# Performance work log

Hardware: AMD Instinct MI355X
Metric: run time of the kernel (lower is better)

## Reference

```python
import jax, jax.numpy as jnp
import numpy as np

N = 100000
E = 1600000
F_IN = 64
DIM = 64
OUT = 2
BN_EPS = 1e-5


def setup_inputs() -> dict:
    key = jax.random.key(0)
    ks = jax.random.split(key, 12)
    s = lambda fan_in: 1.0 / np.sqrt(fan_in)
    inp = {
        "x": jax.random.normal(ks[0], (N, F_IN), dtype=jnp.float32),
        "edge_index": jax.random.randint(ks[1], (2, E), 0, N, dtype=jnp.int64),
        # conv1 MLP: Linear(F_IN, DIM) -> ReLU -> Linear(DIM, DIM)
        "W1a": jax.random.uniform(ks[2], (F_IN, DIM), jnp.float32, -s(F_IN), s(F_IN)),
        "b1a": jnp.zeros((DIM,), jnp.float32),
        "W1b": jax.random.uniform(ks[3], (DIM, DIM), jnp.float32, -s(DIM), s(DIM)),
        "b1b": jnp.zeros((DIM,), jnp.float32),
        "g1": jnp.ones((DIM,), jnp.float32),
        "be1": jnp.zeros((DIM,), jnp.float32),
        # conv5 MLP: Linear(DIM, DIM) -> ReLU -> Linear(DIM, 2)
        "W5a": jax.random.uniform(ks[4], (DIM, DIM), jnp.float32, -s(DIM), s(DIM)),
        "b5a": jnp.zeros((DIM,), jnp.float32),
        "W5b": jax.random.uniform(ks[5], (DIM, OUT), jnp.float32, -s(DIM), s(DIM)),
        "b5b": jnp.zeros((OUT,), jnp.float32),
        "g5": jnp.ones((OUT,), jnp.float32),
        "be5": jnp.zeros((OUT,), jnp.float32),
    }
    return inp


def _gin_agg(x, src, dst):
    # GINConv with eps=0: (1+eps)*x + sum_{j in N(i)} x_j
    agg = jax.ops.segment_sum(x[src], dst, num_segments=N)
    return x + agg


def _batchnorm(h, gamma, beta):
    mu = jnp.mean(h, axis=0)
    var = jnp.var(h, axis=0)  # biased, as torch BN uses for normalization
    return (h - mu) * jax.lax.rsqrt(var + BN_EPS) * gamma + beta


def reference(x, edge_index, W1a, b1a, W1b, b1b, g1, be1,
              W5a, b5a, W5b, b5b, g5, be5):
    src, dst = edge_index[0], edge_index[1]
    # conv1
    h = _gin_agg(x, src, dst)                      # [N, F_IN]
    h = jax.nn.relu(h @ W1a + b1a) @ W1b + b1b     # [N, DIM]
    h = jax.nn.relu(h)
    h = _batchnorm(h, g1, be1)
    # conv5
    h = _gin_agg(h, src, dst)                      # [N, DIM]
    h = jax.nn.relu(h @ W5a + b5a) @ W5b + b5b     # [N, OUT]
    h = jax.nn.relu(h)
    h = _batchnorm(h, g5, be5)
    return h
```

## Files before the change

kernel.cpp:

```cpp
#include <hip/hip_runtime.h>

#define NN 100000
#define FD 64
#define OUTF 2
#define NB 391
#define NBP 392
#define P1CH 4096
#define NTILE 6250
#define MLPB 782
#define GPSTR 800

typedef short bf16x8 __attribute__((ext_vector_type(8), may_alias));
typedef float f32x4 __attribute__((ext_vector_type(4)));
typedef float f32x2 __attribute__((ext_vector_type(2)));

__device__ inline ushort f2bf(float f) {
    uint u = __float_as_uint(f);
    uint r = (u + 0x7FFFu + ((u >> 16) & 1u)) >> 16;
    return (ushort)r;
}
__device__ inline float bf2f(ushort v) {
    return __uint_as_float(((uint)v) << 16);
}


__global__ void k_zero(float* __restrict__ p, int n) {
    int i = blockIdx.x * blockDim.x + threadIdx.x;
    if (i < n) p[i] = 0.f;
}

__global__ void k_copy4(const float4* __restrict__ s, float4* __restrict__ d, int n4) {
    int i = blockIdx.x * blockDim.x + threadIdx.x;
    int st = gridDim.x * blockDim.x;
    for (; i < n4; i += st) d[i] = s[i];
}

__global__ void k_cvt(const float4* __restrict__ x4, ushort4* __restrict__ xb4, int n4) {
    int i = blockIdx.x * blockDim.x + threadIdx.x;
    int st = gridDim.x * blockDim.x;
    for (; i < n4; i += st) {
        float4 v = x4[i];
        ushort4 w;
        w.x = f2bf(v.x);
        w.y = f2bf(v.y);
        w.z = f2bf(v.z);
        w.w = f2bf(v.w);
        xb4[i] = w;
    }
}

__global__ __launch_bounds__(256) void k_cvt_hist(
        const int* __restrict__ ei, int* __restrict__ ghist, int E_, int np1,
        const float4* __restrict__ x4, ushort4* __restrict__ xb4,
        ushort* __restrict__ xb, ushort* __restrict__ h1b, int n4) {
    __shared__ int h[NB];
    int tid = threadIdx.x;
    int blk = blockIdx.x;
    if (blk < np1) {
        for (int i = tid; i < NB; i += 256) h[i] = 0;
        __syncthreads();
        int c0 = blk * P1CH;
        int c1 = min(c0 + P1CH, E_);
        for (int i = c0 + tid; i < c1; i += 256) {
            int d = ei[E_ + i];
            int b = min(max(d >> 8, 0), NB - 1);
            atomicAdd(&h[b], 1);
        }
        __syncthreads();
        int* row = ghist + (size_t)blk * NBP;
        for (int i = tid; i < NB; i += 256) row[i] = h[i];
    } else {
        int bb = blk - np1;
        if (bb == 0 && tid < 16) {
            ushort4 z = {0, 0, 0, 0};
            ((ushort4*)(xb + (size_t)NN * FD))[tid] = z;
            ((ushort4*)(h1b + (size_t)NN * FD))[tid] = z;
        }
        int i = bb * 256 + tid;
        int st = 2048 * 256;
        for (; i < n4; i += st) {
            float4 v = x4[i];
            ushort4 w;
            w.x = f2bf(v.x);
            w.y = f2bf(v.y);
            w.z = f2bf(v.z);
            w.w = f2bf(v.w);
            xb4[i] = w;
        }
    }
}


__global__ __launch_bounds__(512) void k_scanCol(int* __restrict__ ghist,
                                                 int* __restrict__ tot, int np1) {
    __shared__ int ts[512];
    int b = blockIdx.x;
    int tid = threadIdx.x;
    int v = (tid < np1) ? ghist[(size_t)tid * NBP + b] : 0;
    ts[tid] = v;
    __syncthreads();
    for (int off = 1; off < 512; off <<= 1) {
        int u = (tid >= off) ? ts[tid - off] : 0;
        __syncthreads();
        ts[tid] += u;
        __syncthreads();
    }
    if (tid < np1) ghist[(size_t)tid * NBP + b] = ts[tid] - v;
    if (tid == 511) tot[b] = ts[511];
}

__global__ __launch_bounds__(512) void k_scanB2(const int* __restrict__ tot,
                                                int* __restrict__ bbase,
                                                float* __restrict__ S) {
    __shared__ int ts[512];
    int tid = threadIdx.x;
    if (tid < 192) S[tid] = 0.f;
    int v = (tid < NB) ? tot[tid] : 0;
    ts[tid] = v;
    __syncthreads();
    for (int off = 1; off < 512; off <<= 1) {
        int u = (tid >= off) ? ts[tid - off] : 0;
        __syncthreads();
        ts[tid] += u;
        __syncthreads();
    }
    if (tid < NB) bbase[tid] = ts[tid] - v;
    if (tid == 511) bbase[NB] = ts[511];
}

__global__ __launch_bounds__(256) void k_p1b2(const int* __restrict__ ei,
                                              const int* __restrict__ ghist,
                                              const int* __restrict__ bbase,
                                              int* __restrict__ part, int E_) {
    __shared__ int cur[NB];
    int tid = threadIdx.x;
    const int* row = ghist + (size_t)blockIdx.x * NBP;
    for (int i = tid; i < NB; i += 256) cur[i] = bbase[i] + row[i];
    __syncthreads();
    int c0 = blockIdx.x * P1CH;
    int c1 = min(c0 + P1CH, E_);
    for (int i = c0 + tid; i < c1; i += 256) {
        int s = ei[i];
        int d = ei[E_ + i];
        int b = min(max(d >> 8, 0), NB - 1);
        int slot = atomicAdd(&cur[b], 1);
        part[slot] = ((d & 255) << 20) | (s & 0xFFFFF);
    }
}

__global__ __launch_bounds__(256) void k_build(const int* __restrict__ part,
                                               const int* __restrict__ bbase,
                                               int* __restrict__ rowptr,
                                               int* __restrict__ csr, int E_) {
    __shared__ int cnt[256];
    __shared__ int ts[256];
    __shared__ int cur[256];
    int b = blockIdx.x;
    int tid = threadIdx.x;
    cnt[tid] = 0;
    __syncthreads();
    int s0 = bbase[b], s1 = bbase[b + 1];
    for (int i = s0 + tid; i < s1; i += 256) {
        int v = part[i];
        atomicAdd(&cnt[(v >> 20) & 255], 1);
    }
    __syncthreads();
    int v = cnt[tid];
    ts[tid] = v;
    __syncthreads();
    for (int off = 1; off < 256; off <<= 1) {
        int u = (tid >= off) ? ts[tid - off] : 0;
        __syncthreads();
        ts[tid] += u;
        __syncthreads();
    }
    int excl = ts[tid] - v;
    int node = b * 256 + tid;
    if (node < NN) rowptr[node] = s0 + excl;
    cur[tid] = s0 + excl;
    if (b == 0 && tid == 0) rowptr[NN] = E_;
    __syncthreads();
    for (int i = s0 + tid; i < s1; i += 256) {
        int v2 = part[i];
        int lj = (v2 >> 20) & 255;
        int pos = atomicAdd(&cur[lj], 1);
        csr[pos] = v2 & 0xFFFFF;
    }
}


#define GSTEP(T, A01, A23)                                                     \
    {                                                                          \
        int s = __shfl(id, (T) * 4 + g);                                       \
        uint2 v = *(const uint2*)(Xb + ((long)s << 6) + (l << 2));             \
        f32x2 p, q2;                                                           \
        p[0] = __uint_as_float(v.x << 16);                                     \
        p[1] = __uint_as_float(v.x & 0xFFFF0000u);                             \
        q2[0] = __uint_as_float(v.y << 16);                                    \
        q2[1] = __uint_as_float(v.y & 0xFFFF0000u);                            \
        A01 += p;                                                              \
        A23 += q2;                                                             \
    }

__global__ __launch_bounds__(256) void k_gather2(
        const ushort* __restrict__ Xb, const int* __restrict__ rowptr,
        const int* __restrict__ csr,
        const float* __restrict__ bs, const float* __restrict__ bq,
        const float* __restrict__ gam, const float* __restrict__ bet,
        ushort* __restrict__ outb, int affine) {
    int tid = threadIdx.x;
    int lane = tid & 63;
    int n = (blockIdx.x * blockDim.x + tid) >> 6;
    if (n >= NN) return;
    int g = lane >> 4;
    int l = lane & 15;
    int start = rowptr[n], end = rowptr[n + 1];
    int deg = end - start;

    f32x2 a01 = {0.f, 0.f}, a23 = {0.f, 0.f};
    f32x2 b01 = {0.f, 0.f}, b23 = {0.f, 0.f};
    if (g == 0) {
        uint2 v = *(const uint2*)(Xb + ((long)n << 6) + (l << 2));
        a01[0] = __uint_as_float(v.x << 16);
        a01[1] = __uint_as_float(v.x & 0xFFFF0000u);
        a23[0] = __uint_as_float(v.y << 16);
        a23[1] = __uint_as_float(v.y & 0xFFFF0000u);
    }

    for (int base = start; base < end; base += 64) {
        int cnt = min(end - base, 64);
        int id = NN;
        if (lane < cnt) id = csr[base + lane];
        int nsteps = (cnt + 3) >> 2;
        int t = 0;
        for (; t + 4 <= nsteps; t += 4) {
            GSTEP(t + 0, a01, a23)
            GSTEP(t + 1, b01, b23)
            GSTEP(t + 2, a01, a23)
            GSTEP(t + 3, b01, b23)
        }
        for (; t + 2 <= nsteps; t += 2) {
            GSTEP(t + 0, a01, a23)
            GSTEP(t + 1, b01, b23)
        }
        if (t < nsteps) GSTEP(t, a01, a23)
    }
    a01 += b01;
    a23 += b23;
    float A[4] = {a01[0], a01[1], a23[0], a23[1]};
#pragma unroll
    for (int c = 0; c < 4; c++) {
        float v = A[c];
        v += __shfl_xor(v, 16);
        v += __shfl_xor(v, 32);
        A[c] = v;
    }

    if (g == 0) {
        if (affine) {
            float dp1 = (float)(deg + 1);
#pragma unroll
            for (int c = 0; c < 4; c++) {
                int ch = l * 4 + c;
                float mu = bs[ch] * (1.f / NN);
                float var = bq[ch] * (1.f / NN) - mu * mu;
                float s = gam[ch] * rsqrtf(var + 1e-5f);
                float sh = fmaf(-mu, s, bet[ch]);
                A[c] = fmaf(A[c], s, dp1 * sh);
            }
        }
        ushort4 v;
        v.x = f2bf(A[0]); v.y = f2bf(A[1]); v.z = f2bf(A[2]); v.w = f2bf(A[3]);
        ((ushort4*)(outb + ((long)n << 6)))[l] = v;
    }
}


__global__ __launch_bounds__(256) void k_mlp1_mfma(
        const ushort* __restrict__ Ab,
        const float* __restrict__ Wa, const float* __restrict__ ba,
        const float* __restrict__ Wb, const float* __restrict__ bb,
        ushort* __restrict__ H, float* __restrict__ gp1s, float* __restrict__ gp1q) {
    __shared__ __attribute__((aligned(16))) short tile[4][16 * 72];
    __shared__ float sArr[64], qArr[64];
    int tid = threadIdx.x;
    int w = tid >> 6, lane = tid & 63;
    int l = lane & 15, quad = lane >> 4;
    if (tid < 64) { sArr[tid] = 0.f; qArr[tid] = 0.f; }
    __syncthreads();

    bf16x8 B1[2][4], B2[2][4];
#pragma unroll
    for (int ks = 0; ks < 2; ks++)
#pragma unroll
        for (int t = 0; t < 4; t++) {
            bf16x8 f1, f2;
#pragma unroll
            for (int j = 0; j < 8; j++) {
                int k = ks * 32 + quad * 8 + j;
                f1[j] = (short)f2bf(Wa[k * 64 + t * 16 + l]);
                f2[j] = (short)f2bf(Wb[k * 64 + t * 16 + l]);
            }
            B1[ks][t] = f1;
            B2[ks][t] = f2;
        }
    float bias1[4], bias2[4];
#pragma unroll
    for (int t = 0; t < 4; t++) {
        bias1[t] = ba[t * 16 + l];
        bias2[t] = bb[t * 16 + l];
    }

    float s[4] = {0.f, 0.f, 0.f, 0.f}, q[4] = {0.f, 0.f, 0.f, 0.f};
    short* tp = &tile[w][0];
    int gw = blockIdx.x * 4 + w;
    int nw = gridDim.x * 4;
    bf16x8 A0, A1;
    if (gw < NTILE) {
        int m0 = gw * 16;
        A0 = *(const bf16x8*)(Ab + (size_t)(m0 + l) * FD + quad * 8);
        A1 = *(const bf16x8*)(Ab + (size_t)(m0 + l) * FD + 32 + quad * 8);
    }
    for (int tau = gw; tau < NTILE; tau += nw) {
        int m0 = tau * 16;
        int nxt = tau + nw;
        bf16x8 nA0, nA1;
        if (nxt < NTILE) {
            int nm0 = nxt * 16;
            nA0 = *(const bf16x8*)(Ab + (size_t)(nm0 + l) * FD + quad * 8);
            nA1 = *(const bf16x8*)(Ab + (size_t)(nm0 + l) * FD + 32 + quad * 8);
        }
#pragma unroll
        for (int t = 0; t < 4; t++) {
            f32x4 c = {0.f, 0.f, 0.f, 0.f};
            c = __builtin_amdgcn_mfma_f32_16x16x32_bf16(A0, B1[0][t], c, 0, 0, 0);
            c = __builtin_amdgcn_mfma_f32_16x16x32_bf16(A1, B1[1][t], c, 0, 0, 0);
#pragma unroll
            for (int r = 0; r < 4; r++) {
                float v = fmaxf(c[r] + bias1[t], 0.f);
                tp[(quad * 4 + r) * 72 + t * 16 + l] = (short)f2bf(v);
            }
        }
        bf16x8 A20 = *(const bf16x8*)&tp[l * 72 + quad * 8];
        bf16x8 A21 = *(const bf16x8*)&tp[l * 72 + 32 + quad * 8];
#pragma unroll
        for (int t = 0; t < 4; t++) {
            f32x4 c = {0.f, 0.f, 0.f, 0.f};
            c = __builtin_amdgcn_mfma_f32_16x16x32_bf16(A20, B2[0][t], c, 0, 0, 0);
            c = __builtin_amdgcn_mfma_f32_16x16x32_bf16(A21, B2[1][t], c, 0, 0, 0);
#pragma unroll
            for (int r = 0; r < 4; r++) {
                float v = fmaxf(c[r] + bias2[t], 0.f);
                s[t] += v;
                q[t] += v * v;
                tp[(quad * 4 + r) * 72 + t * 16 + l] = (short)f2bf(v);
            }
        }
        int row = lane >> 2, ch = lane & 3;
        bf16x8 o0 = *(const bf16x8*)&tp[row * 72 + ch * 16];
        bf16x8 o1 = *(const bf16x8*)&tp[row * 72 + ch * 16 + 8];
        *(bf16x8*)(H + (size_t)(m0 + row) * FD + ch * 16) = o0;
        *(bf16x8*)(H + (size_t)(m0 + row) * FD + ch * 16 + 8) = o1;
        A0 = nA0;
        A1 = nA1;
    }
#pragma unroll
    for (int t = 0; t < 4; t++) {
        s[t] += __shfl_xor(s[t], 16); s[t] += __shfl_xor(s[t], 32);
        q[t] += __shfl_xor(q[t], 16); q[t] += __shfl_xor(q[t], 32);
    }
    if (quad == 0) {
#pragma unroll
        for (int t = 0; t < 4; t++) {
            atomicAdd(&sArr[t * 16 + l], s[t]);
            atomicAdd(&qArr[t * 16 + l], q[t]);
        }
    }
    __syncthreads();
    if (tid < 64) {
        gp1s[tid * GPSTR + blockIdx.x] = sArr[tid];
        gp1q[tid * GPSTR + blockIdx.x] = qArr[tid];
    }
}

__global__ __launch_bounds__(256) void k_red1(const float* __restrict__ gp1s,
                                              const float* __restrict__ gp1q,
                                              float* __restrict__ gsum,
                                              float* __restrict__ gsq, int nb) {
    __shared__ float rs[256], rq[256];
    int ch = blockIdx.x;
    int tid = threadIdx.x;
    float s = 0.f, q = 0.f;
    for (int k = tid; k < nb; k += 256) {
        s += gp1s[ch * GPSTR + k];
        q += gp1q[ch * GPSTR + k];
    }
    rs[tid] = s;
    rq[tid] = q;
    __syncthreads();
    for (int off = 128; off > 0; off >>= 1) {
        if (tid < off) {
            rs[tid] += rs[tid + off];
            rq[tid] += rq[tid + off];
        }
        __syncthreads();
    }
    if (tid == 0) {
        gsum[ch] = rs[0];
        gsq[ch] = rq[0];
    }
}

__global__ __launch_bounds__(256) void k_mlp2_mfma(
        const ushort* __restrict__ Ab,
        const float* __restrict__ Wa, const float* __restrict__ ba,
        const float* __restrict__ Wb2, const float* __restrict__ bb2,
        float* __restrict__ O, float* __restrict__ gsum, float* __restrict__ gsq) {
    __shared__ __attribute__((aligned(16))) short tile[4][16 * 72];
    __shared__ float sArr[2], qArr[2];
    int tid = threadIdx.x;
    int w = tid >> 6, lane = tid & 63;
    int l = lane & 15, quad = lane >> 4;
    if (tid < 2) { sArr[tid] = 0.f; qArr[tid] = 0.f; }
    __syncthreads();

    bf16x8 B1[2][4], B2[2];
#pragma unroll
    for (int ks = 0; ks < 2; ks++) {
#pragma unroll
        for (int t = 0; t < 4; t++) {
            bf16x8 f1;
#pragma unroll
            for (int j = 0; j < 8; j++) {
                int k = ks * 32 + quad * 8 + j;
                f1[j] = (short)f2bf(Wa[k * 64 + t * 16 + l]);
            }
            B1[ks][t] = f1;
        }
        bf16x8 f2;
#pragma unroll
        for (int j = 0; j < 8; j++) {
            int k = ks * 32 + quad * 8 + j;
            f2[j] = (l < OUTF) ? (short)f2bf(Wb2[k * OUTF + l]) : (short)0;
        }
        B2[ks] = f2;
    }
    float bias1[4];
#pragma unroll
    for (int t = 0; t < 4; t++) bias1[t] = ba[t * 16 + l];
    float bias2 = (l < OUTF) ? bb2[l] : 0.f;

    float s = 0.f, q = 0.f;
    short* tp = &tile[w][0];
    int gw = blockIdx.x * 4 + w;
    int nw = gridDim.x * 4;
    bf16x8 A0, A1;
    if (gw < NTILE) {
        int m0 = gw * 16;
        A0 = *(const bf16x8*)(Ab + (size_t)(m0 + l) * FD + quad * 8);
        A1 = *(const bf16x8*)(Ab + (size_t)(m0 + l) * FD + 32 + quad * 8);
    }
    for (int tau = gw; tau < NTILE; tau += nw) {
        int m0 = tau * 16;
        int nxt = tau + nw;
        bf16x8 nA0, nA1;
        if (nxt < NTILE) {
            int nm0 = nxt * 16;
            nA0 = *(const bf16x8*)(Ab + (size_t)(nm0 + l) * FD + quad * 8);
            nA1 = *(const bf16x8*)(Ab + (size_t)(nm0 + l) * FD + 32 + quad * 8);
        }
#pragma unroll
        for (int t = 0; t < 4; t++) {
            f32x4 c = {0.f, 0.f, 0.f, 0.f};
            c = __builtin_amdgcn_mfma_f32_16x16x32_bf16(A0, B1[0][t], c, 0, 0, 0);
            c = __builtin_amdgcn_mfma_f32_16x16x32_bf16(A1, B1[1][t], c, 0, 0, 0);
#pragma unroll
            for (int r = 0; r < 4; r++) {
                float v = fmaxf(c[r] + bias1[t], 0.f);
                tp[(quad * 4 + r) * 72 + t * 16 + l] = (short)f2bf(v);
            }
        }
        bf16x8 A20 = *(const bf16x8*)&tp[l * 72 + quad * 8];
        bf16x8 A21 = *(const bf16x8*)&tp[l * 72 + 32 + quad * 8];
        f32x4 c = {0.f, 0.f, 0.f, 0.f};
        c = __builtin_amdgcn_mfma_f32_16x16x32_bf16(A20, B2[0], c, 0, 0, 0);
        c = __builtin_amdgcn_mfma_f32_16x16x32_bf16(A21, B2[1], c, 0, 0, 0);
#pragma unroll
        for (int r = 0; r < 4; r++) {
            float v = fmaxf(c[r] + bias2, 0.f);
            if (l < OUTF) {
                s += v;
                q += v * v;
                O[(size_t)(m0 + quad * 4 + r) * OUTF + l] = v;
            }
        }
        A0 = nA0;
        A1 = nA1;
    }
    s += __shfl_xor(s, 16); s += __shfl_xor(s, 32);
    q += __shfl_xor(q, 16); q += __shfl_xor(q, 32);
    if (quad == 0 && l < OUTF) {
        atomicAdd(&sArr[l], s);
        atomicAdd(&qArr[l], q);
    }
    __syncthreads();
    if (tid < OUTF) {
        atomicAdd(&gsum[tid], sArr[tid]);
        atomicAdd(&gsq[tid], qArr[tid]);
    }
}

template <bool BF16OUT>
__global__ __launch_bounds__(256) void k_mlp64(
        const float* __restrict__ X,
        const float* __restrict__ Wa, const float* __restrict__ ba,
        const float* __restrict__ Wb, const float* __restrict__ bb,
        void* __restrict__ Hv, float* __restrict__ gsum, float* __restrict__ gsq) {
    __shared__ float row[256 * 65];
    int tid = threadIdx.x;
    long node = (long)blockIdx.x * 256 + tid;
    bool valid = node < NN;
    if (valid) {
        const float4* rp = (const float4*)(X + node * FD);
#pragma unroll
        for (int q = 0; q < 16; q++) {
            float4 v = rp[q];
            row[tid * 65 + 4 * q + 0] = v.x;
            row[tid * 65 + 4 * q + 1] = v.y;
            row[tid * 65 + 4 * q + 2] = v.z;
            row[tid * 65 + 4 * q + 3] = v.w;
        }
    }
    float acc[64];
#pragma unroll
    for (int j = 0; j < 64; j++) acc[j] = ba[j];
    if (valid) {
        for (int k = 0; k < 64; k++) {
            float xv = row[tid * 65 + k];
            const float* wr = Wa + k * 64;
#pragma unroll
            for (int j = 0; j < 64; j++) acc[j] = fmaf(xv, wr[j], acc[j]);
        }
    }
#pragma unroll
    for (int j = 0; j < 64; j++) row[tid * 65 + j] = fmaxf(acc[j], 0.f);
#pragma unroll
    for (int j = 0; j < 64; j++) acc[j] = bb[j];
    if (valid) {
        for (int k = 0; k < 64; k++) {
            float xv = row[tid * 65 + k];
            const float* wr = Wb + k * 64;
#pragma unroll
            for (int j = 0; j < 64; j++) acc[j] = fmaf(xv, wr[j], acc[j]);
        }
    }
#pragma unroll
    for (int j = 0; j < 64; j++) {
        float v = valid ? fmaxf(acc[j], 0.f) : 0.f;
        row[tid * 65 + j] = v;
    }
    if (valid) {
        if (BF16OUT) {
            ushort4* op = (ushort4*)((ushort*)Hv + node * FD);
#pragma unroll
            for (int q = 0; q < 16; q++) {
                ushort4 w;
                w.x = f2bf(row[tid * 65 + 4 * q + 0]);
                w.y = f2bf(row[tid * 65 + 4 * q + 1]);
                w.z = f2bf(row[tid * 65 + 4 * q + 2]);
                w.w = f2bf(row[tid * 65 + 4 * q + 3]);
                op[q] = w;
            }
        } else {
            float4* op = (float4*)((float*)Hv + node * FD);
#pragma unroll
            for (int q = 0; q < 16; q++) {
                float4 v;
                v.x = row[tid * 65 + 4 * q + 0];
                v.y = row[tid * 65 + 4 * q + 1];
                v.z = row[tid * 65 + 4 * q + 2];
                v.w = row[tid * 65 + 4 * q + 3];
                op[q] = v;
            }
        }
    }
    __syncthreads();
    if (tid < 64) {
        float s = 0.f, q = 0.f;
        for (int r = 0; r < 256; r++) {
            float v = row[r * 65 + tid];
            s += v;
            q += v * v;
        }
        atomicAdd(&gsum[tid], s);
        atomicAdd(&gsq[tid], q);
    }
}

__global__ __launch_bounds__(256) void k_mlp_out(
        const float* __restrict__ X,
        const float* __restrict__ Wa, const float* __restrict__ ba,
        const float* __restrict__ Wb, const float* __restrict__ bb,
        float* __restrict__ O, float* __restrict__ gsum, float* __restrict__ gsq) {
    __shared__ float row[256 * 65];
    __shared__ float red[256][4];
    int tid = threadIdx.x;
    long node = (long)blockIdx.x * 256 + tid;
    bool valid = node < NN;
    if (valid) {
        const float4* rp = (const float4*)(X + node * FD);
#pragma unroll
        for (int q = 0; q < 16; q++) {
            float4 v = rp[q];
            row[tid * 65 + 4 * q + 0] = v.x;
            row[tid * 65 + 4 * q + 1] = v.y;
            row[tid * 65 + 4 * q + 2] = v.z;
            row[tid * 65 + 4 * q + 3] = v.w;
        }
    }
    float acc[64];
#pragma unroll
    for (int j = 0; j < 64; j++) acc[j] = ba[j];
    if (valid) {
        for (int k = 0; k < 64; k++) {
            float xv = row[tid * 65 + k];
            const float* wr = Wa + k * 64;
#pragma unroll
            for (int j = 0; j < 64; j++) acc[j] = fmaf(xv, wr[j], acc[j]);
        }
    }
#pragma unroll
    for (int j = 0; j < 64; j++) row[tid * 65 + j] = fmaxf(acc[j], 0.f);
    float a0 = bb[0];
    float a1 = bb[1];
    if (valid) {
        for (int k = 0; k < 64; k++) {
            float xv = row[tid * 65 + k];
            a0 = fmaf(xv, Wb[k * 2 + 0], a0);
            a1 = fmaf(xv, Wb[k * 2 + 1], a1);
        }
    }
    float v0 = valid ? fmaxf(a0, 0.f) : 0.f;
    float v1 = valid ? fmaxf(a1, 0.f) : 0.f;
    if (valid) {
        float2 v;
        v.x = v0;
        v.y = v1;
        ((float2*)O)[node] = v;
    }
    red[tid][0] = v0;
    red[tid][1] = v0 * v0;
    red[tid][2] = v1;
    red[tid][3] = v1 * v1;
    __syncthreads();
    for (int off = 128; off > 0; off >>= 1) {
        if (tid < off) {
#pragma unroll
            for (int c = 0; c < 4; c++) red[tid][c] += red[tid + off][c];
        }
        __syncthreads();
    }
    if (tid == 0) {
        atomicAdd(&gsum[0], red[0][0]);
        atomicAdd(&gsq[0], red[0][1]);
        atomicAdd(&gsum[1], red[0][2]);
        atomicAdd(&gsq[1], red[0][3]);
    }
}


__global__ void k_bnfin(const float* __restrict__ gsum, const float* __restrict__ gsq,
                        const float* __restrict__ g, const float* __restrict__ be,
                        float* __restrict__ sc, float* __restrict__ sh, int C, float invN) {
    int c = threadIdx.x;
    if (c < C) {
        float mu = gsum[c] * invN;
        float var = gsq[c] * invN - mu * mu;
        float s = g[c] * rsqrtf(var + 1e-5f);
        sc[c] = s;
        sh[c] = fmaf(-mu, s, be[c]);
    }
}

__global__ void k_bnfin_apply2(const float* __restrict__ gsum,
                               const float* __restrict__ gsq,
                               const float* __restrict__ g,
                               const float* __restrict__ be,
                               float* __restrict__ o, int n) {
    int i = blockIdx.x * blockDim.x + threadIdx.x;
    if (i < n) {
        int c = i & 1;
        float mu = gsum[c] * (1.f / NN);
        float var = gsq[c] * (1.f / NN) - mu * mu;
        float s = g[c] * rsqrtf(var + 1e-5f);
        float sh = fmaf(-mu, s, be[c]);
        o[i] = fmaf(o[i], s, sh);
    }
}

__global__ void k_bn_apply2(float* __restrict__ o, const float* __restrict__ sc,
                            const float* __restrict__ sh, int n) {
    int i = blockIdx.x * blockDim.x + threadIdx.x;
    if (i < n) {
        int c = i & 1;
        o[i] = fmaf(o[i], sc[c], sh[c]);
    }
}


__global__ void k_scatter(const float* __restrict__ x, const int* __restrict__ ei,
                          float* __restrict__ agg, int E_) {
    int lane = threadIdx.x & 63;
    int wid = (blockIdx.x * blockDim.x + threadIdx.x) >> 6;
    int nw = (gridDim.x * blockDim.x) >> 6;
    for (long e = wid; e < E_; e += nw) {
        int s = ei[e];
        int d = ei[E_ + e];
        float v = x[(long)s * FD + lane];
        atomicAdd(&agg[(long)d * FD + lane], v);
    }
}

__global__ void k_scatter_bn(const float* __restrict__ h, const int* __restrict__ ei,
                             const float* __restrict__ sc, const float* __restrict__ sh,
                             float* __restrict__ agg, int E_) {
    int lane = threadIdx.x & 63;
    float scl = sc[lane];
    float shf = sh[lane];
    int wid = (blockIdx.x * blockDim.x + threadIdx.x) >> 6;
    int nw = (gridDim.x * blockDim.x) >> 6;
    for (long e = wid; e < E_; e += nw) {
        int s = ei[e];
        int d = ei[E_ + e];
        float v = fmaf(h[(long)s * FD + lane], scl, shf);
        atomicAdd(&agg[(long)d * FD + lane], v);
    }
}

__global__ void k_bn_copy(const float4* __restrict__ h, const float4* __restrict__ sc4,
                          const float4* __restrict__ sh4, float4* __restrict__ o, int n4) {
    int i = blockIdx.x * blockDim.x + threadIdx.x;
    int st = gridDim.x * blockDim.x;
    for (; i < n4; i += st) {
        float4 v = h[i];
        int c = i & 15;
        float4 s = sc4[c];
        float4 b = sh4[c];
        v.x = fmaf(v.x, s.x, b.x);
        v.y = fmaf(v.y, s.y, b.y);
        v.z = fmaf(v.z, s.z, b.z);
        v.w = fmaf(v.w, s.w, b.w);
        o[i] = v;
    }
}


extern "C" void kernel_launch(void* const* d_in, const int* in_sizes, int n_in,
                              void* d_out, int out_size, void* d_ws, size_t ws_size,
                              hipStream_t stream) {
    const float* x   = (const float*)d_in[0];
    const int*   ei  = (const int*)d_in[1];
    const float* W1a = (const float*)d_in[2];
    const float* b1a = (const float*)d_in[3];
    const float* W1b = (const float*)d_in[4];
    const float* b1b = (const float*)d_in[5];
    const float* g1  = (const float*)d_in[6];
    const float* be1 = (const float*)d_in[7];
    const float* W5a = (const float*)d_in[8];
    const float* b5a = (const float*)d_in[9];
    const float* W5b = (const float*)d_in[10];
    const float* b5b = (const float*)d_in[11];
    const float* g5  = (const float*)d_in[12];
    const float* be5 = (const float*)d_in[13];
    float* out = (float*)d_out;

    const int E = in_sizes[1] / 2;

    float* ws = (float*)d_ws;
    float* agg = ws;
    ushort* aggb = (ushort*)ws;
    float* gp1s = ws + 3200000;
    float* gp1q = ws + 3260000;
    ushort* xb  = (ushort*)(ws + 6400000);
    ushort* h1b = (ushort*)(ws + 9600032);
    float* h1_fb = ws + 6400000;
    float* S   = ws + 12800064;
    float* gsum1  = S;
    float* gsq1   = S + 64;
    float* gsum2  = S + 128;
    float* gsq2   = S + 160;
    float* scale1 = S + 192;
    float* shift1 = S + 256;
    float* scale2 = S + 320;
    float* shift2 = S + 328;

    int* ibase  = (int*)(S + 512);
    int* rowptr = ibase;
    int* csr    = ibase + 100004;
    int* bbase  = ibase + 100004 + E;
    int* tot    = bbase + 400;
    int* ghist  = tot + 392;
    int* part   = (int*)agg;

    const int np1 = (E + P1CH - 1) / P1CH;
    size_t needed = (size_t)(12800064 + 512) * 4 +
                    (size_t)(100004 + E + 400 + 392 + (size_t)np1 * NBP) * 4;

    const int n4 = NN * FD / 4;
    const int nblk = (NN + 255) / 256;

    if (ws_size >= needed && np1 <= 512) {
        k_cvt_hist<<<np1 + 2048, 256, 0, stream>>>(ei, ghist, E, np1, (const float4*)x,
                                                   (ushort4*)xb, xb, h1b, n4);
        k_scanCol<<<NB, 512, 0, stream>>>(ghist, tot, np1);
        k_scanB2<<<1, 512, 0, stream>>>(tot, bbase, S);
        k_p1b2<<<np1, 256, 0, stream>>>(ei, ghist, bbase, part, E);
        k_build<<<NB, 256, 0, stream>>>(part, bbase, rowptr, csr, E);

        k_gather2<<<25000, 256, 0, stream>>>(xb, rowptr, csr, nullptr, nullptr,
                                             nullptr, nullptr, aggb, 0);
        k_mlp1_mfma<<<MLPB, 256, 0, stream>>>(aggb, W1a, b1a, W1b, b1b, h1b, gp1s, gp1q);
        k_red1<<<64, 256, 0, stream>>>(gp1s, gp1q, gsum1, gsq1, MLPB);
        k_gather2<<<25000, 256, 0, stream>>>(h1b, rowptr, csr, gsum1, gsq1,
                                             g1, be1, aggb, 1);
        k_mlp2_mfma<<<MLPB, 256, 0, stream>>>(aggb, W5a, b5a, W5b, b5b, out, gsum2, gsq2);
        k_bnfin_apply2<<<(NN * OUTF + 255) / 256, 256, 0, stream>>>(gsum2, gsq2, g5, be5,
                                                                    out, NN * OUTF);
    } else {
        k_zero<<<1, 256, 0, stream>>>(S, 192);
        k_copy4<<<4096, 256, 0, stream>>>((const float4*)x, (float4*)agg, n4);
        k_scatter<<<4096, 256, 0, stream>>>(x, ei, agg, E);
        k_mlp64<false><<<nblk, 256, 0, stream>>>(agg, W1a, b1a, W1b, b1b,
                                                 (void*)h1_fb, gsum1, gsq1);
        k_bnfin<<<1, 64, 0, stream>>>(gsum1, gsq1, g1, be1, scale1, shift1, 64, 1.f / NN);
        k_bn_copy<<<4096, 256, 0, stream>>>((const float4*)h1_fb, (const float4*)scale1,
                                            (const float4*)shift1, (float4*)agg, n4);
        k_scatter_bn<<<4096, 256, 0, stream>>>(h1_fb, ei, scale1, shift1, agg, E);
        k_mlp_out<<<nblk, 256, 0, stream>>>(agg, W5a, b5a, W5b, b5b, out, gsum2, gsq2);
        k_bnfin<<<1, 64, 0, stream>>>(gsum2, gsq2, g5, be5, scale2, shift2, OUTF, 1.f / NN);
        k_bn_apply2<<<(NN * OUTF + 255) / 256, 256, 0, stream>>>(out, scale2, shift2, NN * OUTF);
    }
}
```

Baseline: 263.3 us.

## Fold scan and BN reductions into last-block epilogues; stage bucket edges in LDS

Removes two small kernel launches (k_scanB2 and k_red1) by having the last finishing block of k_scanCol and k_mlp1_mfma, detected through an atomic counter with thread fences, perform the global scan and the per-channel BN reduction. The counters are zeroed in k_cvt_hist. k_build now caches each bucket's edges in a 24KB LDS buffer so the second pass reads LDS instead of global memory. The trade-off is a serialized tail in one block and more LDS per block, which may lower occupancy in k_build.

```diff
diff --git a/kernel.cpp b/kernel.cpp
--- a/kernel.cpp
+++ b/kernel.cpp
@@ -9,6 +9,7 @@
 #define NTILE 6250
 #define MLPB 782
 #define GPSTR 800
+#define BCAP 6016
 
 typedef short bf16x8 __attribute__((ext_vector_type(8), may_alias));
 typedef float f32x4 __attribute__((ext_vector_type(4)));
@@ -52,7 +53,8 @@
 __global__ __launch_bounds__(256) void k_cvt_hist(
         const int* __restrict__ ei, int* __restrict__ ghist, int E_, int np1,
         const float4* __restrict__ x4, ushort4* __restrict__ xb4,
-        ushort* __restrict__ xb, ushort* __restrict__ h1b, int n4) {
+        ushort* __restrict__ xb, ushort* __restrict__ h1b,
+        int* __restrict__ ctrs, int n4) {
     __shared__ int h[NB];
     int tid = threadIdx.x;
     int blk = blockIdx.x;
@@ -76,6 +78,10 @@
             ((ushort4*)(xb + (size_t)NN * FD))[tid] = z;
             ((ushort4*)(h1b + (size_t)NN * FD))[tid] = z;
         }
+        if (bb == 0 && tid == 16) {
+            ctrs[0] = 0;
+            ctrs[1] = 0;
+        }
         int i = bb * 256 + tid;
         int st = 2048 * 256;
         for (; i < n4; i += st) {
@@ -90,10 +96,13 @@
     }
 }
 
-
 __global__ __launch_bounds__(512) void k_scanCol(int* __restrict__ ghist,
-                                                 int* __restrict__ tot, int np1) {
+                                                 int* __restrict__ tot, int np1,
+                                                 int* __restrict__ bbase,
+                                                 float* __restrict__ S,
+                                                 int* __restrict__ ctr) {
     __shared__ int ts[512];
+    __shared__ int isLast;
     int b = blockIdx.x;
     int tid = threadIdx.x;
     int v = (tid < np1) ? ghist[(size_t)tid * NBP + b] : 0;
@@ -107,16 +116,17 @@
     }
     if (tid < np1) ghist[(size_t)tid * NBP + b] = ts[tid] - v;
     if (tid == 511) tot[b] = ts[511];
-}
-
-__global__ __launch_bounds__(512) void k_scanB2(const int* __restrict__ tot,
-                                                int* __restrict__ bbase,
-                                                float* __restrict__ S) {
-    __shared__ int ts[512];
-    int tid = threadIdx.x;
+    __syncthreads();
+    if (tid == 0) {
+        __threadfence();
+        isLast = (atomicAdd(ctr, 1) == NB - 1);
+    }
+    __syncthreads();
+    if (!isLast) return;
+    __threadfence();
     if (tid < 192) S[tid] = 0.f;
-    int v = (tid < NB) ? tot[tid] : 0;
-    ts[tid] = v;
+    int v2 = (tid < NB) ? tot[tid] : 0;
+    ts[tid] = v2;
     __syncthreads();
     for (int off = 1; off < 512; off <<= 1) {
         int u = (tid >= off) ? ts[tid - off] : 0;
@@ -124,7 +134,7 @@
         ts[tid] += u;
         __syncthreads();
     }
-    if (tid < NB) bbase[tid] = ts[tid] - v;
+    if (tid < NB) bbase[tid] = ts[tid] - v2;
     if (tid == 511) bbase[NB] = ts[511];
 }
 
@@ -155,14 +165,25 @@
     __shared__ int cnt[256];
     __shared__ int ts[256];
     __shared__ int cur[256];
+    __shared__ int ebuf[BCAP];
     int b = blockIdx.x;
     int tid = threadIdx.x;
     cnt[tid] = 0;
     __syncthreads();
     int s0 = bbase[b], s1 = bbase[b + 1];
-    for (int i = s0 + tid; i < s1; i += 256) {
-        int v = part[i];
-        atomicAdd(&cnt[(v >> 20) & 255], 1);
+    int len = s1 - s0;
+    bool inLds = (len <= BCAP);
+    if (inLds) {
+        for (int i = tid; i < len; i += 256) {
+            int v = part[s0 + i];
+            ebuf[i] = v;
+            atomicAdd(&cnt[(v >> 20) & 255], 1);
+        }
+    } else {
+        for (int i = tid; i < len; i += 256) {
+            int v = part[s0 + i];
+            atomicAdd(&cnt[(v >> 20) & 255], 1);
+        }
     }
     __syncthreads();
     int v = cnt[tid];
@@ -180,11 +201,20 @@
     cur[tid] = s0 + excl;
     if (b == 0 && tid == 0) rowptr[NN] = E_;
     __syncthreads();
-    for (int i = s0 + tid; i < s1; i += 256) {
-        int v2 = part[i];
-        int lj = (v2 >> 20) & 255;
-        int pos = atomicAdd(&cur[lj], 1);
-        csr[pos] = v2 & 0xFFFFF;
+    if (inLds) {
+        for (int i = tid; i < len; i += 256) {
+            int v2 = ebuf[i];
+            int lj = (v2 >> 20) & 255;
+            int pos = atomicAdd(&cur[lj], 1);
+            csr[pos] = v2 & 0xFFFFF;
+        }
+    } else {
+        for (int i = tid; i < len; i += 256) {
+            int v2 = part[s0 + i];
+            int lj = (v2 >> 20) & 255;
+            int pos = atomicAdd(&cur[lj], 1);
+            csr[pos] = v2 & 0xFFFFF;
+        }
     }
 }
 
@@ -280,9 +310,12 @@
         const ushort* __restrict__ Ab,
         const float* __restrict__ Wa, const float* __restrict__ ba,
         const float* __restrict__ Wb, const float* __restrict__ bb,
-        ushort* __restrict__ H, float* __restrict__ gp1s, float* __restrict__ gp1q) {
+        ushort* __restrict__ H, float* __restrict__ gp1s, float* __restrict__ gp1q,
+        float* __restrict__ gsum, float* __restrict__ gsq, int* __restrict__ ctr) {
     __shared__ __attribute__((aligned(16))) short tile[4][16 * 72];
     __shared__ float sArr[64], qArr[64];
+    __shared__ float rs[256], rq[256];
+    __shared__ int isLast;
     int tid = threadIdx.x;
     int w = tid >> 6, lane = tid & 63;
     int l = lane & 15, quad = lane >> 4;
@@ -381,33 +414,26 @@
         gp1s[tid * GPSTR + blockIdx.x] = sArr[tid];
         gp1q[tid * GPSTR + blockIdx.x] = qArr[tid];
     }
-}
-
-__global__ __launch_bounds__(256) void k_red1(const float* __restrict__ gp1s,
-                                              const float* __restrict__ gp1q,
-                                              float* __restrict__ gsum,
-                                              float* __restrict__ gsq, int nb) {
-    __shared__ float rs[256], rq[256];
-    int ch = blockIdx.x;
-    int tid = threadIdx.x;
-    float s = 0.f, q = 0.f;
-    for (int k = tid; k < nb; k += 256) {
-        s += gp1s[ch * GPSTR + k];
-        q += gp1q[ch * GPSTR + k];
-    }
-    rs[tid] = s;
-    rq[tid] = q;
-    __syncthreads();
-    for (int off = 128; off > 0; off >>= 1) {
-        if (tid < off) {
-            rs[tid] += rs[tid + off];
-            rq[tid] += rq[tid + off];
-        }
-        __syncthreads();
-    }
+    __syncthreads();
     if (tid == 0) {
-        gsum[ch] = rs[0];
-        gsq[ch] = rq[0];
+        __threadfence();
+        isLast = (atomicAdd(ctr, 1) == (int)gridDim.x - 1);
+    }
+    __syncthreads();
+    if (!isLast) return;
+    __threadfence();
+    int ch = tid & 63, seg = tid >> 6;
+    float ss = 0.f, qq = 0.f;
+    for (int k = seg; k < MLPB; k += 4) {
+        ss += gp1s[ch * GPSTR + k];
+        qq += gp1q[ch * GPSTR + k];
+    }
+    rs[tid] = ss;
+    rq[tid] = qq;
+    __syncthreads();
+    if (tid < 64) {
+        gsum[ch] = rs[tid] + rs[tid + 64] + rs[tid + 128] + rs[tid + 192];
+        gsq[ch] = rq[tid] + rq[tid + 64] + rq[tid + 128] + rq[tid + 192];
     }
 }
 
@@ -798,6 +824,7 @@
     int* rowptr = ibase;
     int* csr    = ibase + 100004;
     int* bbase  = ibase + 100004 + E;
+    int* ctrs   = bbase + 396;
     int* tot    = bbase + 400;
     int* ghist  = tot + 392;
     int* part   = (int*)agg;
@@ -811,16 +838,15 @@
 
     if (ws_size >= needed && np1 <= 512) {
         k_cvt_hist<<<np1 + 2048, 256, 0, stream>>>(ei, ghist, E, np1, (const float4*)x,
-                                                   (ushort4*)xb, xb, h1b, n4);
-        k_scanCol<<<NB, 512, 0, stream>>>(ghist, tot, np1);
-        k_scanB2<<<1, 512, 0, stream>>>(tot, bbase, S);
+                                                   (ushort4*)xb, xb, h1b, ctrs, n4);
+        k_scanCol<<<NB, 512, 0, stream>>>(ghist, tot, np1, bbase, S, &ctrs[0]);
         k_p1b2<<<np1, 256, 0, stream>>>(ei, ghist, bbase, part, E);
         k_build<<<NB, 256, 0, stream>>>(part, bbase, rowptr, csr, E);
 
         k_gather2<<<25000, 256, 0, stream>>>(xb, rowptr, csr, nullptr, nullptr,
                                              nullptr, nullptr, aggb, 0);
-        k_mlp1_mfma<<<MLPB, 256, 0, stream>>>(aggb, W1a, b1a, W1b, b1b, h1b, gp1s, gp1q);
-        k_red1<<<64, 256, 0, stream>>>(gp1s, gp1q, gsum1, gsq1, MLPB);
+        k_mlp1_mfma<<<MLPB, 256, 0, stream>>>(aggb, W1a, b1a, W1b, b1b, h1b,
+                                              gp1s, gp1q, gsum1, gsq1, &ctrs[1]);
         k_gather2<<<25000, 256, 0, stream>>>(h1b, rowptr, csr, gsum1, gsq1,
                                              g1, be1, aggb, 1);
         k_mlp2_mfma<<<MLPB, 256, 0, stream>>>(aggb, W5a, b5a, W5b, b5b, out, gsum2, gsq2);
```

New measurement: 356.5 us. 1.35x slower.
